# Kernel optimization log

Hardware: AMD Instinct MI355X
Metric: run time of the kernel (lower is better)

The kernel has to match this reference:

```python
import jax, jax.numpy as jnp
import numpy as np

BETA = 1.0  # lagr_softmax default inverse temperature

def setup_inputs() -> dict:
    key = jax.random.key(0)
    ks = jax.random.split(key, 5)
    B, Tq, Tk, Eq, Ek, E, H = 2, 2048, 2048, 1024, 1024, 1024, 16
    s = lambda d: 1.0 / np.sqrt(d)
    return {
        "gq": jax.random.normal(ks[0], (B, Tq, Eq), jnp.float32),
        "gk": jax.random.normal(ks[1], (B, Tk, Ek), jnp.float32),
        "WQ": jax.random.normal(ks[2], (E, Eq), jnp.float32) * s(Eq),
        "WK": jax.random.normal(ks[3], (E, Ek), jnp.float32) * s(Ek),
        "Wmix": jax.random.normal(ks[4], (1, H), jnp.float32) * s(H),
    }

def reference(gq, gk, WQ, WK, Wmix):
    B, Tq, _ = gq.shape
    H = Wmix.shape[1]
    E = WQ.shape[0]
    D = E // H
    # Linear projections (bias=False): x @ W.T
    q = (gq @ WQ.T).reshape(B, Tq, H, D)          # (B,Tq,H,D)
    k = (gk @ WK.T).reshape(B, -1, H, D)          # (B,Tk,H,D)
    # scores q @ k^T per head: (B,H,Tq,Tk)
    a = jnp.einsum('bqhd,bkhd->bhqk', q, k)
    # mix_heads: Linear(n_heads -> 1) applied over head axis
    a = jnp.einsum('bhqk,h->bqk', a, Wmix[0])     # (B,Tq,Tk)
    # lagr_softmax: (1/beta) * logsumexp(beta * a, dim=-1)
    out = jax.nn.logsumexp(BETA * a, axis=-1) / BETA  # (B,Tq)
    return out[:, None, :]                        # (B,1,Tq) matching torch shape
```

## Files before the change

kernel.cpp:

```cpp
#include <hip/hip_runtime.h>
#include <hip/hip_bf16.h>
#include <math.h>

#define B_    2
#define TQ    2048
#define TK    2048
#define E_    1024
#define MTOT  4096

typedef __attribute__((ext_vector_type(8))) short bf16x8;
typedef __attribute__((ext_vector_type(4))) float f32x4;

__device__ __forceinline__ unsigned short f2bf(float x) {
  unsigned int u = __float_as_uint(x);
  u += 0x7fff + ((u >> 16) & 1);
  return (unsigned short)(u >> 16);
}

__device__ __forceinline__ void load_lds16(const void* g, void* l) {
  __builtin_amdgcn_global_load_lds(
      (const __attribute__((address_space(1))) unsigned int*)g,
      (__attribute__((address_space(3))) unsigned int*)l, 16, 0, 0);
}

#define BARRIER() do { asm volatile("" ::: "memory"); __builtin_amdgcn_s_barrier(); asm volatile("" ::: "memory"); } while (0)
#define WAIT_VM4()   asm volatile("s_waitcnt vmcnt(4)" ::: "memory")
#define WAIT_VM0()   asm volatile("s_waitcnt vmcnt(0)" ::: "memory")


__device__ __forceinline__ void stage_A(const unsigned short* gsrc, unsigned short* lds,
                                        int tid, int kt) {
  const int r  = tid >> 3;
  const int c8 = ((tid & 7) ^ (r & 7)) * 8;
  const unsigned short* g = gsrc + (size_t)r * E_ + (size_t)kt * 64 + c8;
  unsigned short* l = lds + tid * 8;
#pragma unroll
  for (int i = 0; i < 4; ++i)
    load_lds16(g + (size_t)(64 * i) * E_, l + 4096 * i);
}
__device__ __forceinline__ void stage_B(const unsigned short* gsrc, unsigned short* lds,
                                        int tid, int kt) {
  const int r  = tid >> 3;
  const int c8 = ((tid & 7) ^ (r & 7)) * 8;
  const unsigned short* g = gsrc + (size_t)r * E_ + (size_t)kt * 64 + c8;
  unsigned short* l = lds + tid * 8;
#pragma unroll
  for (int i = 0; i < 2; ++i)
    load_lds16(g + (size_t)(64 * i) * E_, l + 4096 * i);
}

#define LDS_AT(base, row, o) ((const bf16x8*)((base) + (((row) * 128 + ((o) ^ (((row) & 7) << 4))) >> 1)))

#define READ_A_ALL()                                                          \
  do {                                                                        \
    _Pragma("unroll") for (int f = 0; f < 4; ++f)                             \
      _Pragma("unroll") for (int ks = 0; ks < 2; ++ks)                        \
        a[f][ks] = *LDS_AT(Ac, wm * 64 + f * 16 + li16, ks * 64 + hi4 * 16);  \
  } while (0)

#define READ_B(g0)                                                            \
  do {                                                                        \
    _Pragma("unroll") for (int g = (g0); g < (g0) + 2; ++g)                   \
      _Pragma("unroll") for (int ks = 0; ks < 2; ++ks)                        \
        b[g][ks] = *LDS_AT(Bc, wn * 64 + g * 16 + li16, ks * 64 + hi4 * 16);  \
  } while (0)

#define MFMA_HALF(g0)                                                         \
  do {                                                                        \
    __builtin_amdgcn_s_setprio(1);                                            \
    _Pragma("unroll") for (int ks = 0; ks < 2; ++ks)                          \
      _Pragma("unroll") for (int f = 0; f < 4; ++f)                           \
        _Pragma("unroll") for (int g = (g0); g < (g0) + 2; ++g)               \
          acc[f][g] = __builtin_amdgcn_mfma_f32_16x16x32_bf16(                \
              a[f][ks], b[g][ks], acc[f][g], 0, 0, 0);                        \
    __builtin_amdgcn_s_setprio(0);                                            \
  } while (0)

#define GEMM_PIPELINE()                                                       \
  do {                                                                        \
    stage_A(Ag, Asl[0], tid, 0);                                              \
    stage_B(Bg, Bsl[0], tid, 0);                                              \
    stage_A(Ag, Asl[1], tid, 1);                                              \
    WAIT_VM4();                   \
    int s0 = 0, s2 = 2;                                     \
    for (int t = 0; t < 16; ++t) {                                            \
      BARRIER();                                                              \
      const unsigned short* Ac = Asl[s0];                                     \
      const unsigned short* Bc = Bsl[t & 1];                                  \
                                                         \
      READ_A_ALL(); READ_B(0);                                                \
      stage_B(Bg, Bsl[(t + 1) & 1], tid, (t + 1) & 15);                       \
      MFMA_HALF(0);                                                           \
                                                        \
      READ_B(2);                                                              \
      stage_A(Ag, Asl[s2], tid, (t + 2) & 15);                                \
      MFMA_HALF(2);                                                           \
      WAIT_VM4();                                                             \
      s0 = (s0 == 2) ? 0 : s0 + 1;                                            \
      s2 = (s2 == 2) ? 0 : s2 + 1;                                            \
    }                                                                         \
  } while (0)

__global__ void prep_kernel(const float* __restrict__ gq, const float* __restrict__ gk,
                            const float* __restrict__ WQ, const float* __restrict__ WK,
                            const float* __restrict__ Wmix,
                            unsigned short* __restrict__ gqb, unsigned short* __restrict__ gkb,
                            unsigned short* __restrict__ wqb, unsigned short* __restrict__ wkb) {
  const int NGQ = (B_ * TQ * E_) / 4;
  const int NW  = (E_ * E_) / 4;
  const int total = 2 * NGQ + 2 * NW;
  for (int idx = blockIdx.x * blockDim.x + threadIdx.x; idx < total;
       idx += gridDim.x * blockDim.x) {
    const float4* src; unsigned short* dst; int local; float scale = 1.0f;
    if (idx < NGQ)            { src = (const float4*)gq; dst = gqb; local = idx; }
    else if (idx < 2 * NGQ)   { src = (const float4*)gk; dst = gkb; local = idx - NGQ; }
    else if (idx < 2*NGQ+NW)  { src = (const float4*)WQ; dst = wqb; local = idx - 2*NGQ;
                                scale = Wmix[local >> 14]; }
    else                      { src = (const float4*)WK; dst = wkb; local = idx - 2*NGQ - NW; }
    float4 v = src[local];
    ushort4 o;
    o.x = f2bf(v.x * scale); o.y = f2bf(v.y * scale);
    o.z = f2bf(v.z * scale); o.w = f2bf(v.w * scale);
    ((ushort4*)dst)[local] = o;
  }
}

__global__ __launch_bounds__(512, 2) void proj_kernel(
    const unsigned short* __restrict__ gqb, const unsigned short* __restrict__ gkb,
    const unsigned short* __restrict__ wqb, const unsigned short* __restrict__ wkb,
    unsigned short* __restrict__ qp, unsigned short* __restrict__ kp) {
  __shared__ __align__(16) unsigned short Asl[3][16384];
  __shared__ __align__(16) unsigned short Bsl[2][8192];
  const int m0 = blockIdx.y * 256, n0 = blockIdx.x * 128;
  const unsigned short* Ag = (blockIdx.z ? gkb : gqb) + (size_t)m0 * E_;
  const unsigned short* Bg = (blockIdx.z ? wkb : wqb) + (size_t)n0 * E_;
  unsigned short* C        = (blockIdx.z ? kp  : qp);
  const int tid = threadIdx.x, wave = tid >> 6, lane = tid & 63;
  const int wm = wave >> 1, wn = wave & 1, li16 = lane & 15, hi4 = lane >> 4;
  f32x4 acc[4][4] = {};
  bf16x8 a[4][2];
  bf16x8 b[4][2];
  GEMM_PIPELINE();
#pragma unroll
  for (int f = 0; f < 4; ++f)
#pragma unroll
    for (int g = 0; g < 4; ++g)
#pragma unroll
      for (int j = 0; j < 4; ++j) {
        int row = m0 + wm * 64 + f * 16 + hi4 * 4 + j;
        int col = n0 + wn * 64 + g * 16 + li16;
        C[(size_t)row * E_ + col] = f2bf(acc[f][g][j]);
      }
  WAIT_VM0();
}

__global__ __launch_bounds__(512, 2) void score_lse_kernel(
    const unsigned short* __restrict__ qp, const unsigned short* __restrict__ kp,
    float2* __restrict__ partials) {
  __shared__ __align__(16) unsigned short Asl[3][16384];
  __shared__ __align__(16) unsigned short Bsl[2][8192];
  __shared__ float redM[2][256];
  __shared__ float redS[2][256];
  const int bb = blockIdx.z;
  const int m0 = blockIdx.y * 256, n0 = blockIdx.x * 128;
  const unsigned short* Ag = qp + (size_t)bb * TQ * E_ + (size_t)m0 * E_;
  const unsigned short* Bg = kp + (size_t)bb * TK * E_ + (size_t)n0 * E_;
  const int tid = threadIdx.x, wave = tid >> 6, lane = tid & 63;
  const int wm = wave >> 1, wn = wave & 1, li16 = lane & 15, hi4 = lane >> 4;
  f32x4 acc[4][4] = {};
  bf16x8 a[4][2];
  bf16x8 b[4][2];
  GEMM_PIPELINE();
#pragma unroll
  for (int f = 0; f < 4; ++f) {
#pragma unroll
    for (int j = 0; j < 4; ++j) {
      float m = fmaxf(fmaxf(acc[f][0][j], acc[f][1][j]),
                      fmaxf(acc[f][2][j], acc[f][3][j]));
#pragma unroll
      for (int msk = 1; msk < 16; msk <<= 1) m = fmaxf(m, __shfl_xor(m, msk, 64));
      float s = 0.f;
#pragma unroll
      for (int g = 0; g < 4; ++g) s += expf(acc[f][g][j] - m);
#pragma unroll
      for (int msk = 1; msk < 16; msk <<= 1) s += __shfl_xor(s, msk, 64);
      if (li16 == 0) {
        int row = wm * 64 + f * 16 + hi4 * 4 + j;
        redM[wn][row] = m;
        redS[wn][row] = s;
      }
    }
  }
  __syncthreads();
  if (tid < 256) {
    float mA = redM[0][tid], mB = redM[1][tid];
    float M = fmaxf(mA, mB);
    float S = redS[0][tid] * expf(mA - M) + redS[1][tid] * expf(mB - M);
    int qrow = bb * TQ + m0 + tid;
    partials[(size_t)qrow * 16 + blockIdx.x] = make_float2(M, S);
  }
}

__global__ void finalize_kernel(const float2* __restrict__ partials, float* __restrict__ out) {
  int r = blockIdx.x * blockDim.x + threadIdx.x;
  if (r >= MTOT) return;
  const float2* p = partials + (size_t)r * 16;
  float M = p[0].x;
#pragma unroll
  for (int i = 1; i < 16; ++i) M = fmaxf(M, p[i].x);
  float S = 0.f;
#pragma unroll
  for (int i = 0; i < 16; ++i) S += p[i].y * expf(p[i].x - M);
  out[r] = logf(S) + M;
}

extern "C" void kernel_launch(void* const* d_in, const int* in_sizes, int n_in,
                              void* d_out, int out_size, void* d_ws, size_t ws_size,
                              hipStream_t stream) {
  const float* gq   = (const float*)d_in[0];
  const float* gk   = (const float*)d_in[1];
  const float* WQ   = (const float*)d_in[2];
  const float* WK   = (const float*)d_in[3];
  const float* Wmix = (const float*)d_in[4];
  float* out = (float*)d_out;

  char* ws = (char*)d_ws;
  unsigned short* gqb = (unsigned short*)(ws);
  unsigned short* gkb = (unsigned short*)(ws + 8388608);
  unsigned short* wqb = (unsigned short*)(ws + 16777216);
  unsigned short* wkb = (unsigned short*)(ws + 18874368);
  unsigned short* qp  = (unsigned short*)(ws + 20971520);
  unsigned short* kp  = (unsigned short*)(ws + 29360128);
  float2* partials    = (float2*)(ws + 37748736);

  hipLaunchKernelGGL(prep_kernel, dim3(1024), dim3(256), 0, stream,
                     gq, gk, WQ, WK, Wmix, gqb, gkb, wqb, wkb);
  hipLaunchKernelGGL(proj_kernel, dim3(8, 16, 2), dim3(512), 0, stream,
                     gqb, gkb, wqb, wkb, qp, kp);
  hipLaunchKernelGGL(score_lse_kernel, dim3(16, 8, 2), dim3(512), 0, stream,
                     qp, kp, partials);
  hipLaunchKernelGGL(finalize_kernel, dim3(16), dim3(256), 0, stream,
                     partials, out);
}
```

Before: 142.2 us.

## Triple-buffer B tiles and remap blocks onto XCDs for L2 locality

Grows the B shared-memory buffer from double to triple buffering so B is prefetched two k-steps ahead like A, with the wait count raised to match. Both GEMM kernels now use a 1D grid whose block index is decoded so that blocks landing on the same XCD share M/N tiles (and batch), aiming to improve L2 reuse of the operand tiles. Shared memory per block increases by 16 KB, which could affect occupancy at two blocks per CU.

```diff
diff --git a/kernel.cpp b/kernel.cpp
--- a/kernel.cpp
+++ b/kernel.cpp
@@ -24,7 +24,7 @@
 }
 
 #define BARRIER() do { asm volatile("" ::: "memory"); __builtin_amdgcn_s_barrier(); asm volatile("" ::: "memory"); } while (0)
-#define WAIT_VM4()   asm volatile("s_waitcnt vmcnt(4)" ::: "memory")
+#define WAIT_VM6()   asm volatile("s_waitcnt vmcnt(6)" ::: "memory")
 #define WAIT_VM0()   asm volatile("s_waitcnt vmcnt(0)" ::: "memory")
 
 
@@ -78,24 +78,23 @@
 
 #define GEMM_PIPELINE()                                                       \
   do {                                                                        \
-    stage_A(Ag, Asl[0], tid, 0);                                              \
-    stage_B(Bg, Bsl[0], tid, 0);                                              \
-    stage_A(Ag, Asl[1], tid, 1);                                              \
-    WAIT_VM4();                   \
+    stage_B(Bg, Bsl[0], tid, 0); stage_A(Ag, Asl[0], tid, 0);                 \
+    stage_B(Bg, Bsl[1], tid, 1); stage_A(Ag, Asl[1], tid, 1);                 \
+    WAIT_VM6();                   \
     int s0 = 0, s2 = 2;                                     \
     for (int t = 0; t < 16; ++t) {                                            \
       BARRIER();                                                              \
       const unsigned short* Ac = Asl[s0];                                     \
-      const unsigned short* Bc = Bsl[t & 1];                                  \
+      const unsigned short* Bc = Bsl[s0];                                     \
                                                          \
       READ_A_ALL(); READ_B(0);                                                \
-      stage_B(Bg, Bsl[(t + 1) & 1], tid, (t + 1) & 15);                       \
+      stage_B(Bg, Bsl[s2], tid, (t + 2) & 15);                                \
       MFMA_HALF(0);                                                           \
                                                         \
       READ_B(2);                                                              \
       stage_A(Ag, Asl[s2], tid, (t + 2) & 15);                                \
       MFMA_HALF(2);                                                           \
-      WAIT_VM4();                                                             \
+      WAIT_VM6();                                                             \
       s0 = (s0 == 2) ? 0 : s0 + 1;                                            \
       s2 = (s2 == 2) ? 0 : s2 + 1;                                            \
     }                                                                         \
@@ -130,11 +129,16 @@
     const unsigned short* __restrict__ wqb, const unsigned short* __restrict__ wkb,
     unsigned short* __restrict__ qp, unsigned short* __restrict__ kp) {
   __shared__ __align__(16) unsigned short Asl[3][16384];
-  __shared__ __align__(16) unsigned short Bsl[2][8192];
-  const int m0 = blockIdx.y * 256, n0 = blockIdx.x * 128;
-  const unsigned short* Ag = (blockIdx.z ? gkb : gqb) + (size_t)m0 * E_;
-  const unsigned short* Bg = (blockIdx.z ? wkb : wqb) + (size_t)n0 * E_;
-  unsigned short* C        = (blockIdx.z ? kp  : qp);
+  __shared__ __align__(16) unsigned short Bsl[3][8192];
+  const int g_  = blockIdx.x;
+  const int xcd = g_ & 7, j = g_ >> 3;
+  const int side = xcd >> 2, r_ = xcd & 3;
+  const int mt = r_ * 4 + (j & 3);
+  const int nt = j >> 2;
+  const int m0 = mt * 256, n0 = nt * 128;
+  const unsigned short* Ag = (side ? gkb : gqb) + (size_t)m0 * E_;
+  const unsigned short* Bg = (side ? wkb : wqb) + (size_t)n0 * E_;
+  unsigned short* C        = (side ? kp  : qp);
   const int tid = threadIdx.x, wave = tid >> 6, lane = tid & 63;
   const int wm = wave >> 1, wn = wave & 1, li16 = lane & 15, hi4 = lane >> 4;
   f32x4 acc[4][4] = {};
@@ -146,10 +150,10 @@
 #pragma unroll
     for (int g = 0; g < 4; ++g)
 #pragma unroll
-      for (int j = 0; j < 4; ++j) {
-        int row = m0 + wm * 64 + f * 16 + hi4 * 4 + j;
+      for (int j2 = 0; j2 < 4; ++j2) {
+        int row = m0 + wm * 64 + f * 16 + hi4 * 4 + j2;
         int col = n0 + wn * 64 + g * 16 + li16;
-        C[(size_t)row * E_ + col] = f2bf(acc[f][g][j]);
+        C[(size_t)row * E_ + col] = f2bf(acc[f][g][j2]);
       }
   WAIT_VM0();
 }
@@ -158,11 +162,15 @@
     const unsigned short* __restrict__ qp, const unsigned short* __restrict__ kp,
     float2* __restrict__ partials) {
   __shared__ __align__(16) unsigned short Asl[3][16384];
-  __shared__ __align__(16) unsigned short Bsl[2][8192];
+  __shared__ __align__(16) unsigned short Bsl[3][8192];
   __shared__ float redM[2][256];
   __shared__ float redS[2][256];
-  const int bb = blockIdx.z;
-  const int m0 = blockIdx.y * 256, n0 = blockIdx.x * 128;
+  const int g_  = blockIdx.x;
+  const int xcd = g_ & 7, j = g_ >> 3;
+  const int bb = xcd >> 2, r_ = xcd & 3;
+  const int qt = (r_ & 1) * 4 + (j & 3);
+  const int kt = (r_ >> 1) * 8 + (j >> 2);
+  const int m0 = qt * 256, n0 = kt * 128;
   const unsigned short* Ag = qp + (size_t)bb * TQ * E_ + (size_t)m0 * E_;
   const unsigned short* Bg = kp + (size_t)bb * TK * E_ + (size_t)n0 * E_;
   const int tid = threadIdx.x, wave = tid >> 6, lane = tid & 63;
@@ -174,18 +182,18 @@
 #pragma unroll
   for (int f = 0; f < 4; ++f) {
 #pragma unroll
-    for (int j = 0; j < 4; ++j) {
-      float m = fmaxf(fmaxf(acc[f][0][j], acc[f][1][j]),
-                      fmaxf(acc[f][2][j], acc[f][3][j]));
+    for (int j2 = 0; j2 < 4; ++j2) {
+      float m = fmaxf(fmaxf(acc[f][0][j2], acc[f][1][j2]),
+                      fmaxf(acc[f][2][j2], acc[f][3][j2]));
 #pragma unroll
       for (int msk = 1; msk < 16; msk <<= 1) m = fmaxf(m, __shfl_xor(m, msk, 64));
       float s = 0.f;
 #pragma unroll
-      for (int g = 0; g < 4; ++g) s += expf(acc[f][g][j] - m);
+      for (int g = 0; g < 4; ++g) s += expf(acc[f][g][j2] - m);
 #pragma unroll
       for (int msk = 1; msk < 16; msk <<= 1) s += __shfl_xor(s, msk, 64);
       if (li16 == 0) {
-        int row = wm * 64 + f * 16 + hi4 * 4 + j;
+        int row = wm * 64 + f * 16 + hi4 * 4 + j2;
         redM[wn][row] = m;
         redS[wn][row] = s;
       }
@@ -197,7 +205,7 @@
     float M = fmaxf(mA, mB);
     float S = redS[0][tid] * expf(mA - M) + redS[1][tid] * expf(mB - M);
     int qrow = bb * TQ + m0 + tid;
-    partials[(size_t)qrow * 16 + blockIdx.x] = make_float2(M, S);
+    partials[(size_t)qrow * 16 + kt] = make_float2(M, S);
   }
 }
 
@@ -235,9 +243,9 @@
 
   hipLaunchKernelGGL(prep_kernel, dim3(1024), dim3(256), 0, stream,
                      gq, gk, WQ, WK, Wmix, gqb, gkb, wqb, wkb);
-  hipLaunchKernelGGL(proj_kernel, dim3(8, 16, 2), dim3(512), 0, stream,
+  hipLaunchKernelGGL(proj_kernel, dim3(256), dim3(512), 0, stream,
                      gqb, gkb, wqb, wkb, qp, kp);
-  hipLaunchKernelGGL(score_lse_kernel, dim3(16, 8, 2), dim3(512), 0, stream,
+  hipLaunchKernelGGL(score_lse_kernel, dim3(256), dim3(512), 0, stream,
                      qp, kp, partials);
   hipLaunchKernelGGL(finalize_kernel, dim3(16), dim3(256), 0, stream,
                      partials, out);
```

New measurement: 132.0 us. 7.2% less time.
